# Kernel optimization log

Measured on AMD Instinct MI355X. Metric: run time of the kernel, lower is better.

Reference implementation:

```python
import jax, jax.numpy as jnp
import numpy as np

N_NODES = 100000
N_EDGES = 1600000
IN_CH, OUT_CH, EDGE_DIM = 128, 64, 32


def setup_inputs() -> dict:
    key = jax.random.key(0)
    ks = jax.random.split(key, 6)
    x = jax.random.normal(ks[0], (N_NODES, IN_CH), dtype=jnp.float32)
    edge_index = jax.random.randint(ks[1], (2, N_EDGES), 0, N_NODES, dtype=jnp.int64)
    edge_attr = jax.random.normal(ks[2], (N_EDGES, EDGE_DIM), dtype=jnp.float32)
    # xavier_uniform bounds: sqrt(6/(fan_in+fan_out))
    bn = float(np.sqrt(6.0 / (IN_CH + OUT_CH)))
    be = float(np.sqrt(6.0 / (EDGE_DIM + OUT_CH)))
    W_node = jax.random.uniform(ks[3], (IN_CH, OUT_CH), minval=-bn, maxval=bn, dtype=jnp.float32)
    W_edge = jax.random.uniform(ks[4], (EDGE_DIM, OUT_CH), minval=-be, maxval=be, dtype=jnp.float32)
    b_node = jnp.zeros((OUT_CH,), dtype=jnp.float32)
    b_edge = jnp.zeros((OUT_CH,), dtype=jnp.float32)
    return {"x": x, "edge_index": edge_index, "edge_attr": edge_attr,
            "W_node": W_node, "b_node": b_node, "W_edge": W_edge, "b_edge": b_edge}


def reference(x, edge_index, edge_attr, W_node, b_node, W_edge, b_edge):
    n = x.shape[0]
    h = x @ W_node + b_node                       # [N, out]
    e = edge_attr @ W_edge + b_edge               # [E, out]
    row, col = edge_index[0], edge_index[1]
    msg = h[col] + e                              # gather + edge add, [E, out]
    s = jax.ops.segment_sum(msg, row, num_segments=n)
    cnt = jax.ops.segment_sum(jnp.ones((msg.shape[0],), dtype=msg.dtype), row, num_segments=n)
    # mean reduce; isolated nodes (count 0) yield 0, matching torch_scatter
    out = s / jnp.maximum(cnt, 1.0)[:, None]
    return out
```

## Files before the change

### kernel.cpp

```cpp
#include <hip/hip_runtime.h>
#include <hip/hip_bf16.h>


#define EPB 4096
#define NBMAX 1024
#define CAPB 2816
#define GEMM_ROWS 32

__global__ __launch_bounds__(256) void init_k(int* __restrict__ bcur, int NB) {
  const int i = blockIdx.x * blockDim.x + threadIdx.x;
  if (i < NB) bcur[i] = i * CAPB;
}

__global__ __launch_bounds__(256) void fused1_k(
    const int* __restrict__ ei, unsigned long long* __restrict__ temp,
    int* __restrict__ bcur, int E, int NB, int P1B,
    const float* __restrict__ x, const float* __restrict__ W,
    const float* __restrict__ b, __hip_bfloat16* __restrict__ h, int N) {
  __shared__ __align__(16) char smem[49152];
  const int t = threadIdx.x;
  if (blockIdx.x < P1B) {
    int* hist = (int*)smem;
    int* base = hist + NBMAX;
    for (int i = t; i < NB; i += 256) hist[i] = 0;
    __syncthreads();
    const int e0 = blockIdx.x * EPB;
    int rows[16];
#pragma unroll
    for (int i = 0; i < 16; ++i) {
      const int e = e0 + i * 256 + t;
      rows[i] = (e < E) ? ei[e] : -1;
      if (rows[i] >= 0) atomicAdd(&hist[rows[i] >> 7], 1);
    }
    __syncthreads();
    for (int i = t; i < NB; i += 256) {
      const int c = hist[i];
      base[i] = c ? atomicAdd(&bcur[i], c) : 0;
      hist[i] = 0;
    }
    __syncthreads();
#pragma unroll
    for (int i = 0; i < 16; ++i) {
      if (rows[i] < 0) continue;
      const int e = e0 + i * 256 + t;
      const unsigned long long col =
          (unsigned long long)(unsigned int)ei[(size_t)E + e];
      const int bk = rows[i] >> 7;
      const int pos = base[bk] + atomicAdd(&hist[bk], 1);
      if (pos < (bk + 1) * CAPB)
        temp[pos] = ((unsigned long long)(rows[i] & 127) << 38) |
                    ((unsigned long long)(unsigned int)e << 17) | col;
    }
  } else {
    float* xl = (float*)smem;
    float* wl = xl + GEMM_ROWS * 128;
    const int bid = blockIdx.x - P1B;
    for (int i = t; i < 128 * 64 / 4; i += 256)
      ((float4*)wl)[i] = ((const float4*)W)[i];
    const int r0 = bid * GEMM_ROWS;
    for (int i = t; i < GEMM_ROWS * 32; i += 256) {
      const int rr = i >> 5;
      const int kk = i & 31;
      const int gr = (r0 + rr < N) ? (r0 + rr) : (N - 1);
      ((float4*)xl)[i] = ((const float4*)(x + (size_t)gr * 128))[kk];
    }
    __syncthreads();
    const int c = t & 63;
    const int wv = t >> 6;
    const float bias = b[c];
    float acc[8];
#pragma unroll
    for (int i = 0; i < 8; ++i) acc[i] = bias;
#pragma unroll 2
    for (int k = 0; k < 128; k += 4) {
      const float w0 = wl[(k + 0) * 64 + c];
      const float w1 = wl[(k + 1) * 64 + c];
      const float w2 = wl[(k + 2) * 64 + c];
      const float w3 = wl[(k + 3) * 64 + c];
#pragma unroll
      for (int i = 0; i < 8; ++i) {
        const float4 x4 = *(const float4*)&xl[(wv * 8 + i) * 128 + k];
        acc[i] = fmaf(x4.x, w0, acc[i]);
        acc[i] = fmaf(x4.y, w1, acc[i]);
        acc[i] = fmaf(x4.z, w2, acc[i]);
        acc[i] = fmaf(x4.w, w3, acc[i]);
      }
    }
#pragma unroll
    for (int i = 0; i < 8; ++i) {
      const int r = r0 + wv * 8 + i;
      if (r < N) h[(size_t)r * 64 + c] = __float2bfloat16(acc[i]);
    }
  }
}

__global__ __launch_bounds__(256) void part2_k(
    const unsigned long long* __restrict__ temp, const int* __restrict__ bcur,
    unsigned long long* __restrict__ list,
    int* __restrict__ offs, int* __restrict__ deg, int N, int NB) {
  __shared__ int cnt[128];
  __shared__ int sd[128];
  __shared__ int lcur[128];
  __shared__ int pre[256];
  const int b = blockIdx.x;
  const int t = threadIdx.x;
  const int r0 = b << 7;
  int ps = 0;
  for (int i = t; i < b; i += 256)
    ps += min(bcur[i], (i + 1) * CAPB) - i * CAPB;
  pre[t] = ps;
  if (t < 128) cnt[t] = 0;
  __syncthreads();
  for (int off = 128; off > 0; off >>= 1) {
    if (t < off) pre[t] += pre[t + off];
    __syncthreads();
  }
  const int bb = pre[0];
  const int start = b * CAPB;
  const int end = min(bcur[b], start + CAPB);
  for (int i = start + t; i < end; i += 256)
    atomicAdd(&cnt[(int)(temp[i] >> 38)], 1);
  __syncthreads();
  if (t < 128) sd[t] = cnt[t];
  __syncthreads();
  for (int off = 1; off < 128; off <<= 1) {
    int val = 0, add = 0;
    if (t < 128) { val = sd[t]; add = (t >= off) ? sd[t - off] : 0; }
    __syncthreads();
    if (t < 128) sd[t] = val + add;
    __syncthreads();
  }
  if (t < 128) {
    const int gbase = bb + sd[t] - cnt[t];
    lcur[t] = gbase;
    const int r = r0 + t;
    if (r < N) { offs[r] = gbase; deg[r] = cnt[t]; }
  }
  __syncthreads();
  for (int i = start + t; i < end; i += 256) {
    const unsigned long long ent = temp[i];
    const int rl = (int)(ent >> 38);
    const int pos = atomicAdd(&lcur[rl], 1);
    list[pos] = ent;
  }
}

__global__ __launch_bounds__(256) void gather_k(
    const unsigned long long* __restrict__ list, const int* __restrict__ offs,
    const int* __restrict__ degv, const unsigned int* __restrict__ h2,
    const float* __restrict__ attr, const float* __restrict__ We,
    const float* __restrict__ be, float* __restrict__ out, int N) {
  __shared__ float wl[32 * 64];
  for (int i = threadIdx.x; i < 32 * 64 / 4; i += 256)
    ((float4*)wl)[i] = ((const float4*)We)[i];
  __syncthreads();
  const int lane = threadIdx.x & 63;
  const int l32 = lane & 31;
  const int node = blockIdx.x * 4 + (threadIdx.x >> 6);
  if (node >= N) return;
  const int base = __builtin_amdgcn_readfirstlane(offs[node]);
  const int deg  = __builtin_amdgcn_readfirstlane(degv[node]);
  float acc0 = 0.f, acc1 = 0.f, acca = 0.f;
  for (int j = 0; j < deg; j += 16) {
    unsigned int dh[16];
    float da[16];
#pragma unroll
    for (int u = 0; u < 16; ++u) {
      if (j + u < deg) {
        const unsigned long long e2 = list[base + j + u];
        const int lo = __builtin_amdgcn_readfirstlane((int)(unsigned int)e2);
        const int hi = __builtin_amdgcn_readfirstlane((int)(unsigned int)(e2 >> 32));
        const int col = lo & 0x1FFFF;
        const int eid = ((unsigned int)lo >> 17) | ((hi & 0x3F) << 15);
        dh[u] = h2[(size_t)col * 32 + l32];
        da[u] = attr[(size_t)eid * 32 + l32];
      } else {
        dh[u] = 0u; da[u] = 0.f;
      }
    }
#pragma unroll
    for (int u = 0; u < 16; ++u) {
      acc0 += __uint_as_float(dh[u] << 16);
      acc1 += __uint_as_float(dh[u] & 0xffff0000u);
      acca += da[u];
    }
  }
  const float ev = __shfl(acc0, lane >> 1);
  const float ov = __shfl(acc1, lane >> 1);
  const float accc = (lane & 1) ? ov : ev;
  float r = 0.f;
#pragma unroll
  for (int k = 0; k < 32; ++k)
    r += __shfl(acca, k) * wl[k * 64 + lane];
  const float cn = (float)deg;
  out[(size_t)node * 64 + lane] = (accc + r + cn * be[lane]) / fmaxf(cn, 1.0f);
}

extern "C" void kernel_launch(void* const* d_in, const int* in_sizes, int n_in,
                              void* d_out, int out_size, void* d_ws, size_t ws_size,
                              hipStream_t stream) {
  const float* x    = (const float*)d_in[0];
  const int*   ei   = (const int*)d_in[1];
  const float* attr = (const float*)d_in[2];
  const float* Wn   = (const float*)d_in[3];
  const float* bn   = (const float*)d_in[4];
  const float* We   = (const float*)d_in[5];
  const float* be   = (const float*)d_in[6];
  float* out = (float*)d_out;

  const int N = in_sizes[0] / 128;
  const int E = in_sizes[2] / 32;
  const int NB = (N + 127) >> 7;

  __hip_bfloat16* h = (__hip_bfloat16*)d_ws;
  unsigned long long* list = (unsigned long long*)((char*)d_ws + ((size_t)N * 64 * 2 + 255) / 256 * 256);
  unsigned long long* temp = list + (size_t)E;
  int* deg   = (int*)(temp + (size_t)NB * CAPB);
  int* offs  = deg + N;
  int* bcur  = offs + N;

  const int P1B = (E + EPB - 1) / EPB;
  const int G2  = (N + GEMM_ROWS - 1) / GEMM_ROWS;

  init_k<<<(NB + 255) / 256, 256, 0, stream>>>(bcur, NB);
  fused1_k<<<P1B + G2, 256, 0, stream>>>(ei, temp, bcur, E, NB, P1B,
                                         x, Wn, bn, h, N);
  part2_k<<<NB, 256, 0, stream>>>(temp, bcur, list, offs, deg, N, NB);
  gather_k<<<(N + 3) / 4, 256, 0, stream>>>(list, offs, deg,
                                            (const unsigned int*)h,
                                            attr, We, be, out, N);
}
```

Baseline: 184.1 us.

## Fuse bucket sort-by-row and gather into one kernel using LDS edge list

Merges the per-bucket counting sort and the gather/mean kernel into a single 512-thread kernel per 128-node bucket. The sorted edge list is kept in shared memory instead of being written to and re-read from global memory, and the global prefix sum over buckets is no longer needed. This removes one launch and the round trip through global memory for the list and the offs/deg arrays. In exchange, only NB (~782) blocks run, each doing the gather for 128 nodes with 8 waves, which lowers parallelism and occupancy. Each block also uses about 23KB of LDS.

Result: no change. 181.9 us (-1.2%).

```diff
diff --git a/kernel.cpp b/kernel.cpp
--- a/kernel.cpp
+++ b/kernel.cpp
@@ -6,6 +6,7 @@
 #define NBMAX 1024
 #define CAPB 2816
 #define GEMM_ROWS 32
+#define FBT 512
 
 __global__ __launch_bounds__(256) void init_k(int* __restrict__ bcur, int NB) {
   const int i = blockIdx.x * blockDim.x + threadIdx.x;
@@ -94,31 +95,27 @@
   }
 }
 
-__global__ __launch_bounds__(256) void part2_k(
+__global__ __launch_bounds__(FBT) void fused2_k(
     const unsigned long long* __restrict__ temp, const int* __restrict__ bcur,
-    unsigned long long* __restrict__ list,
-    int* __restrict__ offs, int* __restrict__ deg, int N, int NB) {
+    const unsigned int* __restrict__ h2, const float* __restrict__ attr,
+    const float* __restrict__ We, const float* __restrict__ be,
+    float* __restrict__ out, int N) {
+  __shared__ float wl[32 * 64];
+  __shared__ unsigned long long llist[CAPB];
   __shared__ int cnt[128];
   __shared__ int sd[128];
+  __shared__ int loff[128];
   __shared__ int lcur[128];
-  __shared__ int pre[256];
   const int b = blockIdx.x;
   const int t = threadIdx.x;
   const int r0 = b << 7;
-  int ps = 0;
-  for (int i = t; i < b; i += 256)
-    ps += min(bcur[i], (i + 1) * CAPB) - i * CAPB;
-  pre[t] = ps;
+  for (int i = t; i < 32 * 64 / 4; i += FBT)
+    ((float4*)wl)[i] = ((const float4*)We)[i];
   if (t < 128) cnt[t] = 0;
   __syncthreads();
-  for (int off = 128; off > 0; off >>= 1) {
-    if (t < off) pre[t] += pre[t + off];
-    __syncthreads();
-  }
-  const int bb = pre[0];
   const int start = b * CAPB;
   const int end = min(bcur[b], start + CAPB);
-  for (int i = start + t; i < end; i += 256)
+  for (int i = start + t; i < end; i += FBT)
     atomicAdd(&cnt[(int)(temp[i] >> 38)], 1);
   __syncthreads();
   if (t < 128) sd[t] = cnt[t];
@@ -131,69 +128,61 @@
     __syncthreads();
   }
   if (t < 128) {
-    const int gbase = bb + sd[t] - cnt[t];
-    lcur[t] = gbase;
-    const int r = r0 + t;
-    if (r < N) { offs[r] = gbase; deg[r] = cnt[t]; }
-  }
-  __syncthreads();
-  for (int i = start + t; i < end; i += 256) {
+    const int o = sd[t] - cnt[t];
+    loff[t] = o;
+    lcur[t] = o;
+  }
+  __syncthreads();
+  for (int i = start + t; i < end; i += FBT) {
     const unsigned long long ent = temp[i];
     const int rl = (int)(ent >> 38);
     const int pos = atomicAdd(&lcur[rl], 1);
-    list[pos] = ent;
-  }
-}
-
-__global__ __launch_bounds__(256) void gather_k(
-    const unsigned long long* __restrict__ list, const int* __restrict__ offs,
-    const int* __restrict__ degv, const unsigned int* __restrict__ h2,
-    const float* __restrict__ attr, const float* __restrict__ We,
-    const float* __restrict__ be, float* __restrict__ out, int N) {
-  __shared__ float wl[32 * 64];
-  for (int i = threadIdx.x; i < 32 * 64 / 4; i += 256)
-    ((float4*)wl)[i] = ((const float4*)We)[i];
-  __syncthreads();
-  const int lane = threadIdx.x & 63;
+    llist[pos] = ent;
+  }
+  __syncthreads();
+  const int lane = t & 63;
   const int l32 = lane & 31;
-  const int node = blockIdx.x * 4 + (threadIdx.x >> 6);
-  if (node >= N) return;
-  const int base = __builtin_amdgcn_readfirstlane(offs[node]);
-  const int deg  = __builtin_amdgcn_readfirstlane(degv[node]);
-  float acc0 = 0.f, acc1 = 0.f, acca = 0.f;
-  for (int j = 0; j < deg; j += 16) {
-    unsigned int dh[16];
-    float da[16];
-#pragma unroll
-    for (int u = 0; u < 16; ++u) {
-      if (j + u < deg) {
-        const unsigned long long e2 = list[base + j + u];
-        const int lo = __builtin_amdgcn_readfirstlane((int)(unsigned int)e2);
-        const int hi = __builtin_amdgcn_readfirstlane((int)(unsigned int)(e2 >> 32));
-        const int col = lo & 0x1FFFF;
-        const int eid = ((unsigned int)lo >> 17) | ((hi & 0x3F) << 15);
-        dh[u] = h2[(size_t)col * 32 + l32];
-        da[u] = attr[(size_t)eid * 32 + l32];
-      } else {
-        dh[u] = 0u; da[u] = 0.f;
+  const int wid = t >> 6;
+  for (int nl = wid; nl < 128; nl += FBT / 64) {
+    const int node = r0 + nl;
+    if (node >= N) break;
+    const int base = __builtin_amdgcn_readfirstlane(loff[nl]);
+    const int deg  = __builtin_amdgcn_readfirstlane(cnt[nl]);
+    float acc0 = 0.f, acc1 = 0.f, acca = 0.f;
+    for (int j = 0; j < deg; j += 16) {
+      unsigned int dh[16];
+      float da[16];
+#pragma unroll
+      for (int u = 0; u < 16; ++u) {
+        if (j + u < deg) {
+          const unsigned long long e2 = llist[base + j + u];
+          const int lo = __builtin_amdgcn_readfirstlane((int)(unsigned int)e2);
+          const int hi = __builtin_amdgcn_readfirstlane((int)(unsigned int)(e2 >> 32));
+          const int col = lo & 0x1FFFF;
+          const int eid = ((unsigned int)lo >> 17) | ((hi & 0x3F) << 15);
+          dh[u] = h2[(size_t)col * 32 + l32];
+          da[u] = attr[(size_t)eid * 32 + l32];
+        } else {
+          dh[u] = 0u; da[u] = 0.f;
+        }
       }
-    }
-#pragma unroll
-    for (int u = 0; u < 16; ++u) {
-      acc0 += __uint_as_float(dh[u] << 16);
-      acc1 += __uint_as_float(dh[u] & 0xffff0000u);
-      acca += da[u];
-    }
-  }
-  const float ev = __shfl(acc0, lane >> 1);
-  const float ov = __shfl(acc1, lane >> 1);
-  const float accc = (lane & 1) ? ov : ev;
-  float r = 0.f;
-#pragma unroll
-  for (int k = 0; k < 32; ++k)
-    r += __shfl(acca, k) * wl[k * 64 + lane];
-  const float cn = (float)deg;
-  out[(size_t)node * 64 + lane] = (accc + r + cn * be[lane]) / fmaxf(cn, 1.0f);
+#pragma unroll
+      for (int u = 0; u < 16; ++u) {
+        acc0 += __uint_as_float(dh[u] << 16);
+        acc1 += __uint_as_float(dh[u] & 0xffff0000u);
+        acca += da[u];
+      }
+    }
+    const float ev = __shfl(acc0, lane >> 1);
+    const float ov = __shfl(acc1, lane >> 1);
+    const float accc = (lane & 1) ? ov : ev;
+    float r = 0.f;
+#pragma unroll
+    for (int k = 0; k < 32; ++k)
+      r += __shfl(acca, k) * wl[k * 64 + lane];
+    const float cn = (float)deg;
+    out[(size_t)node * 64 + lane] = (accc + r + cn * be[lane]) / fmaxf(cn, 1.0f);
+  }
 }
 
 extern "C" void kernel_launch(void* const* d_in, const int* in_sizes, int n_in,
@@ -213,11 +202,8 @@
   const int NB = (N + 127) >> 7;
 
   __hip_bfloat16* h = (__hip_bfloat16*)d_ws;
-  unsigned long long* list = (unsigned long long*)((char*)d_ws + ((size_t)N * 64 * 2 + 255) / 256 * 256);
-  unsigned long long* temp = list + (size_t)E;
-  int* deg   = (int*)(temp + (size_t)NB * CAPB);
-  int* offs  = deg + N;
-  int* bcur  = offs + N;
+  unsigned long long* temp = (unsigned long long*)((char*)d_ws + ((size_t)N * 64 * 2 + 255) / 256 * 256);
+  int* bcur = (int*)(temp + (size_t)NB * CAPB);
 
   const int P1B = (E + EPB - 1) / EPB;
   const int G2  = (N + GEMM_ROWS - 1) / GEMM_ROWS;
@@ -225,8 +211,6 @@
   init_k<<<(NB + 255) / 256, 256, 0, stream>>>(bcur, NB);
   fused1_k<<<P1B + G2, 256, 0, stream>>>(ei, temp, bcur, E, NB, P1B,
                                          x, Wn, bn, h, N);
-  part2_k<<<NB, 256, 0, stream>>>(temp, bcur, list, offs, deg, N, NB);
-  gather_k<<<(N + 3) / 4, 256, 0, stream>>>(list, offs, deg,
-                                            (const unsigned int*)h,
-                                            attr, We, be, out, N);
-}
+  fused2_k<<<NB, FBT, 0, stream>>>(temp, bcur, (const unsigned int*)h,
+                                   attr, We, be, out, N);
+}
```
